# Performance work log

Measured on AMD Instinct MI355X. Metric: run time of the kernel, lower is better.

## Reference

```python
import jax, jax.numpy as jnp
import numpy as np

IN_F = 1024
OUT_F = 1024
GRID_SIZE = 8
GRID_LO, GRID_HI = -2.0, 2.0


def _grid_and_inv_denom():
    grid = jnp.linspace(GRID_LO, GRID_HI, GRID_SIZE)  # [G]
    inv_denom = 1.0 / (float((GRID_HI - GRID_LO) / (GRID_SIZE - 1)) + 1e-06)
    return grid, inv_denom


def setup_inputs() -> dict:
    key = jax.random.key(0)
    kx, kw, ks = jax.random.split(key, 3)
    x = jax.random.normal(kx, (4, 2048, IN_F), dtype=jnp.float32)
    # kaiming_uniform_(a=sqrt(5)) on [out,in]: bound = sqrt(6/((1+a^2)*fan_in)) = sqrt(1/fan_in)
    bound = float(np.sqrt(1.0 / IN_F))
    base_w = jax.random.uniform(kw, (OUT_F, IN_F), minval=-bound, maxval=bound, dtype=jnp.float32)
    base_b = jnp.zeros((OUT_F,), dtype=jnp.float32)
    spline_w = 0.02 * jax.random.normal(ks, (OUT_F, IN_F, GRID_SIZE), dtype=jnp.float32)
    return {"x": x, "base_w": base_w, "base_b": base_b, "spline_w": spline_w}


def reference(x, base_w, base_b, spline_w):
    grid, inv_denom = _grid_and_inv_denom()
    lead = x.shape[:-1]
    x_flat = x.reshape(-1, IN_F)  # [B, in]
    # base path: Linear(SiLU(x))
    base_out = jax.nn.silu(x_flat) @ base_w.T + base_b  # [B, out]
    # RBF basis expansion: [B, in, G]
    basis = jnp.exp(-(((x_flat[..., None] - grid) * inv_denom) ** 2))
    spline_out = jnp.einsum('big,oig->bo', basis, spline_w)  # [B, out]
    out = base_out + spline_out
    return out.reshape(*lead, OUT_F)
```

## Files before the change

kernel.cpp:

```cpp
#include <hip/hip_runtime.h>
#include <stdint.h>

namespace {

constexpr int IN_F = 1024;
constexpr int OUT_F = 1024;
constexpr int GSZ = 8;
constexpr int KTOT = IN_F + IN_F * GSZ;
constexpr int BK = 64;
constexpr int NT = KTOT / BK;
constexpr int NBASE = IN_F / BK;

constexpr int BM = 64, BN = 256;
constexpr int NBLK = OUT_F / BN;
constexpr size_t IMG_BYTES = (size_t)BN * BK * 2;
constexpr size_t WS_NEEDED = (size_t)NBLK * NT * IMG_BYTES;

constexpr double H_D     = 4.0 / 7.0;
constexpr double INVD_D  = 1.0 / (H_D + 1e-6);
constexpr double L2E_D   = 1.4426950408889634;
constexpr double SQL2E_D = 1.2011224087864498;
constexpr double CS_D    = INVD_D * SQL2E_D;
constexpr double DLT_D   = H_D * CS_D;

using short8 = __attribute__((ext_vector_type(8))) short;
using f32x4  = __attribute__((ext_vector_type(4))) float;

__device__ __forceinline__ unsigned cvt_pk(float lo, float hi) {
  unsigned r;
  asm("v_cvt_pk_bf16_f32 %0, %1, %2" : "=v"(r) : "v"(lo), "v"(hi));
  return r;
}
__device__ __forceinline__ float silu_f(float v) {
  float e = __builtin_amdgcn_exp2f(-v * (float)L2E_D);
  return v * __builtin_amdgcn_rcpf(1.0f + e);
}
__device__ __forceinline__ int swz(int row, int kk) {
  return (row * 128 + kk * 2) ^ ((row & 7) << 4);
}

__global__ void wprep(const float* __restrict__ bw, const float* __restrict__ sw,
                      char* __restrict__ wimg)
{
  const int total = NBLK * NT * BN * 8;
  for (int idx = blockIdx.x * blockDim.x + threadIdx.x; idx < total;
       idx += gridDim.x * blockDim.x) {
    const int kk8  = idx & 7;
    const int row  = (idx >> 3) & (BN - 1);
    const int rest = idx >> 11;
    const int step = rest % NT;
    const int nb   = rest / NT;
    const int o    = nb * BN + row;
    const int k    = step * BK + kk8 * 8;
    const float* src = (k < IN_F)
      ? (bw + (size_t)o * IN_F + k)
      : (sw + (size_t)o * (size_t)(IN_F * GSZ) + (k - IN_F));
    const float4 a = ((const float4*)src)[0];
    const float4 b = ((const float4*)src)[1];
    int4 v;
    v.x = (int)cvt_pk(a.x, a.y);
    v.y = (int)cvt_pk(a.z, a.w);
    v.z = (int)cvt_pk(b.x, b.y);
    v.w = (int)cvt_pk(b.z, b.w);
    *(int4*)(wimg + (size_t)rest * IMG_BYTES + swz(row, kk8 * 8)) = v;
  }
}

__global__ __launch_bounds__(256, 2)
void kan_fast(const float* __restrict__ x, const float* __restrict__ bb,
              const char* __restrict__ wimg, float* __restrict__ out)
{
  __shared__ char tA[2][BM * BK * 2];

  const int t    = threadIdx.x;
  const int lane = t & 63;
  const int wid  = t >> 6;
  const int wc   = wid * 64;

  const int d   = blockIdx.x;
  const int r8  = d & 7;
  const int nb  = r8 >> 1;
  const int my  = ((d >> 3) << 1) | (r8 & 1);
  const int bm0 = my * BM;
  const int bn0 = nb * BN;
  const char* img = wimg + (size_t)nb * NT * IMG_BYTES;

  const float CSf  = (float)CS_D;
  const float C0f  = (float)(-2.0 * CS_D);
  const float TDLT = (float)(2.0 * DLT_D);
  float Kc[7];
#pragma unroll
  for (int g = 0; g < 7; ++g) {
    const double cg  = (-2.0 + g * H_D) * CS_D;
    const double cg1 = (-2.0 + (g + 1) * H_D) * CS_D;
    Kc[g] = __builtin_amdgcn_exp2f((float)(-DLT_D * (cg + cg1)));
  }

  f32x4 acc[4][4];
#pragma unroll
  for (int m = 0; m < 4; ++m)
#pragma unroll
    for (int n = 0; n < 4; ++n) acc[m][n] = (f32x4)0.0f;

  const int fr = lane & 15;
  const int kq = (lane >> 4) * 8;

  int boff[8];
#pragma unroll
  for (int n = 0; n < 4; ++n)
#pragma unroll
    for (int kh = 0; kh < 2; ++kh)
      boff[n * 2 + kh] = swz(wc + n * 16 + fr, kh * 32 + kq);

  short8 bE[8], bO[8];
  float4 xE[4], xO[4];

  auto issue_B = [&](int step, short8 (&br)[8]) {
    const char* base = img + (size_t)step * IMG_BYTES;
#pragma unroll
    for (int j = 0; j < 8; ++j)
      br[j] = *(const short8*)(base + boff[j]);
  };

  const int prow = t >> 2;
  const int pcol = t & 3;

  auto load_x = [&](int step, float4 (&xr)[4]) {
    const int k0 = step * BK;
    if (k0 < IN_F) {
      const float* p = x + (size_t)(bm0 + prow) * IN_F + k0 + pcol * 16;
#pragma unroll
      for (int j = 0; j < 4; ++j) xr[j] = ((const float4*)p)[j];
    } else {
      const int i0 = (k0 - IN_F) >> 3;
      const float2 v = *(const float2*)(x + (size_t)(bm0 + prow) * IN_F + i0 + pcol * 2);
      xr[0].x = v.x; xr[0].y = v.y;
    }
  };

  auto conv_A = [&](int step, const float4 (&xr)[4], char* dstA) {
    if (step < NBASE) {
      unsigned q[8];
#pragma unroll
      for (int j = 0; j < 4; ++j) {
        q[2 * j]     = cvt_pk(silu_f(xr[j].x), silu_f(xr[j].y));
        q[2 * j + 1] = cvt_pk(silu_f(xr[j].z), silu_f(xr[j].w));
      }
      const int kc0 = pcol * 16;
      *(int4*)(dstA + swz(prow, kc0))     = make_int4(q[0], q[1], q[2], q[3]);
      *(int4*)(dstA + swz(prow, kc0 + 8)) = make_int4(q[4], q[5], q[6], q[7]);
    } else {
#pragma unroll
      for (int c = 0; c < 2; ++c) {
        const float xv = c ? xr[0].y : xr[0].x;
        const float tb = xv * CSf;
        const float d0 = tb - C0f;
        float e = __builtin_amdgcn_exp2f(-(d0 * d0));
        const float r = __builtin_amdgcn_exp2f(tb * TDLT);
        unsigned q[4];
#pragma unroll
        for (int g = 0; g < 4; ++g) {
          const float a = e;
          const float b = a * r * Kc[2 * g];
          q[g] = cvt_pk(a, b);
          if (g < 3) e = b * r * Kc[2 * g + 1];
        }
        *(int4*)(dstA + swz(prow, (pcol * 2 + c) * 8)) = make_int4(q[0], q[1], q[2], q[3]);
      }
    }
  };

  auto step_body = [&](int s, char* curA, char* nxtA,
                       short8 (&bCur)[8], short8 (&bNxt)[8],
                       const float4 (&xconv)[4], float4 (&xload)[4]) {
    if (s + 1 < NT) issue_B(s + 1, bNxt);
    if (s + 2 < NT) load_x(s + 2, xload);
    if (s + 1 < NT) conv_A(s + 1, xconv, nxtA);
    short8 af[4];
#pragma unroll
    for (int m = 0; m < 4; ++m)
      af[m] = *(const short8*)(curA + swz(m * 16 + fr, kq));
#pragma unroll
    for (int m = 0; m < 4; ++m)
#pragma unroll
      for (int n = 0; n < 4; ++n)
        acc[m][n] = __builtin_amdgcn_mfma_f32_16x16x32_bf16(af[m], bCur[n * 2], acc[m][n], 0, 0, 0);
#pragma unroll
    for (int m = 0; m < 4; ++m)
      af[m] = *(const short8*)(curA + swz(m * 16 + fr, 32 + kq));
#pragma unroll
    for (int m = 0; m < 4; ++m)
#pragma unroll
      for (int n = 0; n < 4; ++n)
        acc[m][n] = __builtin_amdgcn_mfma_f32_16x16x32_bf16(af[m], bCur[n * 2 + 1], acc[m][n], 0, 0, 0);
    __syncthreads();
  };

  load_x(0, xE);
  load_x(1, xO);
  issue_B(0, bE);
  conv_A(0, xE, tA[0]);
  __syncthreads();

  for (int s = 0; s < NT; s += 2) {
    step_body(s,     tA[0], tA[1], bE, bO, xO, xE);
    step_body(s + 1, tA[1], tA[0], bO, bE, xE, xO);
  }

  const int col = lane & 15;
  const int rr  = (lane >> 4) * 4;
#pragma unroll
  for (int m = 0; m < 4; ++m) {
    const int gr = bm0 + m * 16 + rr;
#pragma unroll
    for (int n = 0; n < 4; ++n) {
      const int gc = bn0 + wc + n * 16 + col;
      const float bias = bb[gc];
#pragma unroll
      for (int j = 0; j < 4; ++j)
        out[(size_t)(gr + j) * OUT_F + gc] = acc[m][n][j] + bias;
    }
  }
}

constexpr int SLDK = 64 + 8;

__device__ __forceinline__ unsigned f2bf(float f) {
  unsigned u = __float_as_uint(f);
  return (u + 0x7fffu + ((u >> 16) & 1u)) >> 16;
}
__device__ __forceinline__ unsigned pk2(float lo, float hi) {
  return f2bf(lo) | (f2bf(hi) << 16);
}

__global__ __launch_bounds__(256)
void kan_slow(const float* __restrict__ x, const float* __restrict__ bw,
              const float* __restrict__ bb, const float* __restrict__ sw,
              float* __restrict__ out)
{
  __shared__ unsigned short tA[128][SLDK];
  __shared__ unsigned short tB[128][SLDK];

  const int t    = threadIdx.x;
  const int lane = t & 63;
  const int wid  = t >> 6;
  const int wr   = (wid >> 1) * 64;
  const int wc   = (wid & 1) * 64;
  const int bm0  = blockIdx.x * 128;
  const int bn0  = blockIdx.y * 128;

  const float CS = (float)CS_D;
  float gsc[GSZ];
#pragma unroll
  for (int g = 0; g < GSZ; ++g)
    gsc[g] = (float)((-2.0 + g * H_D) * CS_D);

  f32x4 acc[4][4];
#pragma unroll
  for (int m = 0; m < 4; ++m)
#pragma unroll
    for (int n = 0; n < 4; ++n) acc[m][n] = (f32x4)0.0f;

  float4 rA[8], rB[8];
  const int rw = t >> 4;
  const int cw = (t & 15) * 4;

  auto load_tile = [&](int step) {
    const int k0 = step * BK;
    const bool base = (k0 < IN_F);
#pragma unroll
    for (int j = 0; j < 8; ++j) {
      const int row = j * 16 + rw;
      const float* p = base
        ? (bw + (size_t)(bn0 + row) * IN_F + k0 + cw)
        : (sw + (size_t)(bn0 + row) * (size_t)(IN_F * GSZ) + (k0 - IN_F) + cw);
      rB[j] = *(const float4*)p;
    }
    if (base) {
#pragma unroll
      for (int j = 0; j < 8; ++j) {
        const int row = j * 16 + rw;
        rA[j] = *(const float4*)(x + (size_t)(bm0 + row) * IN_F + k0 + cw);
      }
    } else {
      const int i0  = (k0 - IN_F) >> 3;
      const int row = t >> 1;
      rA[0] = *(const float4*)(x + (size_t)(bm0 + row) * IN_F + i0 + (t & 1) * 4);
    }
  };

  auto store_tile = [&](int step) {
    const int k0 = step * BK;
    const bool base = (k0 < IN_F);
#pragma unroll
    for (int j = 0; j < 8; ++j) {
      const int row = j * 16 + rw;
      uint2 v;
      v.x = pk2(rB[j].x, rB[j].y);
      v.y = pk2(rB[j].z, rB[j].w);
      *(uint2*)&tB[row][cw] = v;
    }
    if (base) {
#pragma unroll
      for (int j = 0; j < 8; ++j) {
        const int row = j * 16 + rw;
        uint2 v;
        v.x = pk2(silu_f(rA[j].x), silu_f(rA[j].y));
        v.y = pk2(silu_f(rA[j].z), silu_f(rA[j].w));
        *(uint2*)&tA[row][cw] = v;
      }
    } else {
      const int row  = t >> 1;
      const int half = t & 1;
      const float* xv = (const float*)&rA[0];
#pragma unroll
      for (int c = 0; c < 4; ++c) {
        const float tb = xv[c] * CS;
        union { unsigned u[4]; int4 v4; } pkv;
#pragma unroll
        for (int g = 0; g < 8; g += 2) {
          const float t0 = tb - gsc[g];
          const float t1 = tb - gsc[g + 1];
          const float e0 = __builtin_amdgcn_exp2f(-(t0 * t0));
          const float e1 = __builtin_amdgcn_exp2f(-(t1 * t1));
          pkv.u[g >> 1] = pk2(e0, e1);
        }
        const int kc = (half * 4 + c) * 8;
        *(int4*)&tA[row][kc] = pkv.v4;
      }
    }
  };

  auto compute_tile = [&]() {
    const int r  = lane & 15;
    const int kq = (lane >> 4) * 8;
#pragma unroll
    for (int kh = 0; kh < 2; ++kh) {
      short8 af[4], bf[4];
#pragma unroll
      for (int m = 0; m < 4; ++m)
        af[m] = *(const short8*)&tA[wr + m * 16 + r][kh * 32 + kq];
#pragma unroll
      for (int n = 0; n < 4; ++n)
        bf[n] = *(const short8*)&tB[wc + n * 16 + r][kh * 32 + kq];
#pragma unroll
      for (int m = 0; m < 4; ++m)
#pragma unroll
        for (int n = 0; n < 4; ++n)
          acc[m][n] = __builtin_amdgcn_mfma_f32_16x16x32_bf16(af[m], bf[n], acc[m][n], 0, 0, 0);
    }
  };

  load_tile(0);
  for (int step = 0; step < NT; ++step) {
    store_tile(step);
    __syncthreads();
    if (step + 1 < NT) load_tile(step + 1);
    compute_tile();
    __syncthreads();
  }

  const int col = lane & 15;
  const int rr  = (lane >> 4) * 4;
#pragma unroll
  for (int m = 0; m < 4; ++m) {
    const int gr = bm0 + wr + m * 16 + rr;
#pragma unroll
    for (int n = 0; n < 4; ++n) {
      const int gc = bn0 + wc + n * 16 + col;
      const float bias = bb[gc];
#pragma unroll
      for (int j = 0; j < 4; ++j)
        out[(size_t)(gr + j) * OUT_F + gc] = acc[m][n][j] + bias;
    }
  }
}

}

extern "C" void kernel_launch(void* const* d_in, const int* in_sizes, int n_in,
                              void* d_out, int out_size, void* d_ws, size_t ws_size,
                              hipStream_t stream) {
  const float *x, *bw, *bb, *sw;
  if (in_sizes[0] == OUT_F) {
    bb = (const float*)d_in[0];
    bw = (const float*)d_in[1];
    sw = (const float*)d_in[2];
    x  = (const float*)d_in[3];
  } else {
    x  = (const float*)d_in[0];
    bw = (const float*)d_in[1];
    bb = (const float*)d_in[2];
    sw = (const float*)d_in[3];
  }
  float* out = (float*)d_out;
  const int rows = (in_sizes[0] == OUT_F) ? in_sizes[3] / IN_F : in_sizes[0] / IN_F;

  if (ws_size >= WS_NEEDED && d_ws != nullptr && (rows % (2 * BM)) == 0) {
    hipLaunchKernelGGL(wprep, dim3(2048), dim3(256), 0, stream, bw, sw, (char*)d_ws);
    const int nblocks = NBLK * (rows / BM);
    hipLaunchKernelGGL(kan_fast, dim3(nblocks), dim3(256), 0, stream,
                       x, bb, (const char*)d_ws, out);
  } else {
    dim3 grid(rows / 128, OUT_F / 128);
    hipLaunchKernelGGL(kan_slow, grid, dim3(256), 0, stream, x, bw, bb, sw, out);
  }
}
```

Before: 191.2 us.

## Use 512-thread blocks with 8 waves each owning 32 output columns

Doubles threads per block to 512 and halves each wave's N tile from 64 to 32 columns. This cuts accumulator and B-register use so more waves can be resident per CU, with launch bounds of 4 blocks per CU. The A-tile conversion is split across twice as many threads, and the register double-buffering of B fragments is dropped in favor of loading B at the start of each step. It also raises wave priority with s_setprio around the MFMA section. In exchange, B-load latency is less hidden and each wave reuses its A fragments over fewer MFMAs, so LDS traffic per MFMA goes up.

```diff
diff --git a/kernel.cpp b/kernel.cpp
--- a/kernel.cpp
+++ b/kernel.cpp
@@ -66,7 +66,7 @@
   }
 }
 
-__global__ __launch_bounds__(256, 2)
+__global__ __launch_bounds__(512, 4)
 void kan_fast(const float* __restrict__ x, const float* __restrict__ bb,
               const char* __restrict__ wimg, float* __restrict__ out)
 {
@@ -75,7 +75,7 @@
   const int t    = threadIdx.x;
   const int lane = t & 63;
   const int wid  = t >> 6;
-  const int wc   = wid * 64;
+  const int wc   = wid * 32;
 
   const int d   = blockIdx.x;
   const int r8  = d & 7;
@@ -96,115 +96,109 @@
     Kc[g] = __builtin_amdgcn_exp2f((float)(-DLT_D * (cg + cg1)));
   }
 
-  f32x4 acc[4][4];
+  f32x4 acc[4][2];
 #pragma unroll
   for (int m = 0; m < 4; ++m)
 #pragma unroll
-    for (int n = 0; n < 4; ++n) acc[m][n] = (f32x4)0.0f;
+    for (int n = 0; n < 2; ++n) acc[m][n] = (f32x4)0.0f;
 
   const int fr = lane & 15;
   const int kq = (lane >> 4) * 8;
 
-  int boff[8];
-#pragma unroll
-  for (int n = 0; n < 4; ++n)
+  int boff[4];
+#pragma unroll
+  for (int n = 0; n < 2; ++n)
 #pragma unroll
     for (int kh = 0; kh < 2; ++kh)
       boff[n * 2 + kh] = swz(wc + n * 16 + fr, kh * 32 + kq);
-
-  short8 bE[8], bO[8];
-  float4 xE[4], xO[4];
-
-  auto issue_B = [&](int step, short8 (&br)[8]) {
-    const char* base = img + (size_t)step * IMG_BYTES;
-#pragma unroll
-    for (int j = 0; j < 8; ++j)
-      br[j] = *(const short8*)(base + boff[j]);
-  };
-
-  const int prow = t >> 2;
-  const int pcol = t & 3;
-
-  auto load_x = [&](int step, float4 (&xr)[4]) {
+  int aoff[8];
+#pragma unroll
+  for (int m = 0; m < 4; ++m)
+#pragma unroll
+    for (int kh = 0; kh < 2; ++kh)
+      aoff[m * 2 + kh] = swz(m * 16 + fr, kh * 32 + kq);
+
+  float4 xE[2], xO[2];
+
+  const int prow = t >> 3;
+  const int pcol = t & 7;
+
+  auto load_x = [&](int step, float4 (&xr)[2]) {
     const int k0 = step * BK;
     if (k0 < IN_F) {
-      const float* p = x + (size_t)(bm0 + prow) * IN_F + k0 + pcol * 16;
-#pragma unroll
-      for (int j = 0; j < 4; ++j) xr[j] = ((const float4*)p)[j];
+      const float* p = x + (size_t)(bm0 + prow) * IN_F + k0 + pcol * 8;
+      xr[0] = ((const float4*)p)[0];
+      xr[1] = ((const float4*)p)[1];
     } else {
       const int i0 = (k0 - IN_F) >> 3;
-      const float2 v = *(const float2*)(x + (size_t)(bm0 + prow) * IN_F + i0 + pcol * 2);
-      xr[0].x = v.x; xr[0].y = v.y;
-    }
-  };
-
-  auto conv_A = [&](int step, const float4 (&xr)[4], char* dstA) {
+      xr[0].x = x[(size_t)(bm0 + prow) * IN_F + i0 + pcol];
+    }
+  };
+
+  auto conv_A = [&](int step, const float4 (&xr)[2], char* dstA) {
+    char* dst = dstA + swz(prow, pcol * 8);
     if (step < NBASE) {
-      unsigned q[8];
-#pragma unroll
-      for (int j = 0; j < 4; ++j) {
-        q[2 * j]     = cvt_pk(silu_f(xr[j].x), silu_f(xr[j].y));
-        q[2 * j + 1] = cvt_pk(silu_f(xr[j].z), silu_f(xr[j].w));
+      unsigned q0 = cvt_pk(silu_f(xr[0].x), silu_f(xr[0].y));
+      unsigned q1 = cvt_pk(silu_f(xr[0].z), silu_f(xr[0].w));
+      unsigned q2 = cvt_pk(silu_f(xr[1].x), silu_f(xr[1].y));
+      unsigned q3 = cvt_pk(silu_f(xr[1].z), silu_f(xr[1].w));
+      *(int4*)dst = make_int4(q0, q1, q2, q3);
+    } else {
+      const float tb = xr[0].x * CSf;
+      const float d0 = tb - C0f;
+      float e = __builtin_amdgcn_exp2f(-(d0 * d0));
+      const float r = __builtin_amdgcn_exp2f(tb * TDLT);
+      unsigned q[4];
+#pragma unroll
+      for (int g = 0; g < 4; ++g) {
+        const float a = e;
+        const float b = a * r * Kc[2 * g];
+        q[g] = cvt_pk(a, b);
+        if (g < 3) e = b * r * Kc[2 * g + 1];
       }
-      const int kc0 = pcol * 16;
-      *(int4*)(dstA + swz(prow, kc0))     = make_int4(q[0], q[1], q[2], q[3]);
-      *(int4*)(dstA + swz(prow, kc0 + 8)) = make_int4(q[4], q[5], q[6], q[7]);
-    } else {
-#pragma unroll
-      for (int c = 0; c < 2; ++c) {
-        const float xv = c ? xr[0].y : xr[0].x;
-        const float tb = xv * CSf;
-        const float d0 = tb - C0f;
-        float e = __builtin_amdgcn_exp2f(-(d0 * d0));
-        const float r = __builtin_amdgcn_exp2f(tb * TDLT);
-        unsigned q[4];
-#pragma unroll
-        for (int g = 0; g < 4; ++g) {
-          const float a = e;
-          const float b = a * r * Kc[2 * g];
-          q[g] = cvt_pk(a, b);
-          if (g < 3) e = b * r * Kc[2 * g + 1];
-        }
-        *(int4*)(dstA + swz(prow, (pcol * 2 + c) * 8)) = make_int4(q[0], q[1], q[2], q[3]);
-      }
-    }
-  };
-
-  auto step_body = [&](int s, char* curA, char* nxtA,
-                       short8 (&bCur)[8], short8 (&bNxt)[8],
-                       const float4 (&xconv)[4], float4 (&xload)[4]) {
-    if (s + 1 < NT) issue_B(s + 1, bNxt);
+      *(int4*)dst = make_int4(q[0], q[1], q[2], q[3]);
+    }
+  };
+
+  auto step_body = [&](int s, const char* curA, char* nxtA,
+                       const float4 (&xconv)[2], float4 (&xload)[2]) {
+    short8 br[4];
+    const char* bbase = img + (size_t)s * IMG_BYTES;
+#pragma unroll
+    for (int j = 0; j < 4; ++j)
+      br[j] = *(const short8*)(bbase + boff[j]);
     if (s + 2 < NT) load_x(s + 2, xload);
     if (s + 1 < NT) conv_A(s + 1, xconv, nxtA);
     short8 af[4];
+    __builtin_amdgcn_s_setprio(1);
 #pragma unroll
     for (int m = 0; m < 4; ++m)
-      af[m] = *(const short8*)(curA + swz(m * 16 + fr, kq));
+      af[m] = *(const short8*)(curA + aoff[m * 2]);
 #pragma unroll
     for (int m = 0; m < 4; ++m)
 #pragma unroll
-      for (int n = 0; n < 4; ++n)
-        acc[m][n] = __builtin_amdgcn_mfma_f32_16x16x32_bf16(af[m], bCur[n * 2], acc[m][n], 0, 0, 0);
+      for (int n = 0; n < 2; ++n)
+        acc[m][n] = __builtin_amdgcn_mfma_f32_16x16x32_bf16(af[m], br[n * 2], acc[m][n], 0, 0, 0);
 #pragma unroll
     for (int m = 0; m < 4; ++m)
-      af[m] = *(const short8*)(curA + swz(m * 16 + fr, 32 + kq));
+      af[m] = *(const short8*)(curA + aoff[m * 2 + 1]);
 #pragma unroll
     for (int m = 0; m < 4; ++m)
 #pragma unroll
-      for (int n = 0; n < 4; ++n)
-        acc[m][n] = __builtin_amdgcn_mfma_f32_16x16x32_bf16(af[m], bCur[n * 2 + 1], acc[m][n], 0, 0, 0);
+      for (int n = 0; n < 2; ++n)
+        acc[m][n] = __builtin_amdgcn_mfma_f32_16x16x32_bf16(af[m], br[n * 2 + 1], acc[m][n], 0, 0, 0);
+    __builtin_amdgcn_s_setprio(0);
     __syncthreads();
   };
 
   load_x(0, xE);
   load_x(1, xO);
-  issue_B(0, bE);
   conv_A(0, xE, tA[0]);
   __syncthreads();
 
   for (int s = 0; s < NT; s += 2) {
-    step_body(s,     tA[0], tA[1], bE, bO, xO, xE);
-    step_body(s + 1, tA[1], tA[0], bO, bE, xE, xO);
+    step_body(s,     tA[0], tA[1], xO, xE);
+    step_body(s + 1, tA[1], tA[0], xE, xO);
   }
 
   const int col = lane & 15;
@@ -213,7 +207,7 @@
   for (int m = 0; m < 4; ++m) {
     const int gr = bm0 + m * 16 + rr;
 #pragma unroll
-    for (int n = 0; n < 4; ++n) {
+    for (int n = 0; n < 2; ++n) {
       const int gc = bn0 + wc + n * 16 + col;
       const float bias = bb[gc];
 #pragma unroll
@@ -399,7 +393,7 @@
   if (ws_size >= WS_NEEDED && d_ws != nullptr && (rows % (2 * BM)) == 0) {
     hipLaunchKernelGGL(wprep, dim3(2048), dim3(256), 0, stream, bw, sw, (char*)d_ws);
     const int nblocks = NBLK * (rows / BM);
-    hipLaunchKernelGGL(kan_fast, dim3(nblocks), dim3(256), 0, stream,
+    hipLaunchKernelGGL(kan_fast, dim3(nblocks), dim3(512), 0, stream,
                        x, bb, (const char*)d_ws, out);
   } else {
     dim3 grid(rows / 128, OUT_F / 128);
```

New measurement: 209.4 us. +9.5%, slower.

## Double block M tile to 128 with 8 waves and stage B in LDS via direct loads

Applied to the files above, without the earlier changes.

Raises the M tile to 128 rows and the block to 512 threads (2x4 waves), so each block reuses every weight tile for twice as many rows and total weight traffic is halved. B tiles now go straight into double-buffered LDS through global_load_lds instead of per-wave register loads. Hand-written waitcnt/barrier handling and setprio around the MFMA section replace __syncthreads to overlap loads with compute. In exchange LDS use grows, the grid holds half as many blocks, and correctness depends on the manual vmcnt counts matching the loads actually issued.

```diff
diff --git a/kernel.cpp b/kernel.cpp
--- a/kernel.cpp
+++ b/kernel.cpp
@@ -11,7 +11,7 @@
 constexpr int NT = KTOT / BK;
 constexpr int NBASE = IN_F / BK;
 
-constexpr int BM = 64, BN = 256;
+constexpr int BM = 128, BN = 256;
 constexpr int NBLK = OUT_F / BN;
 constexpr size_t IMG_BYTES = (size_t)BN * BK * 2;
 constexpr size_t WS_NEEDED = (size_t)NBLK * NT * IMG_BYTES;
@@ -66,21 +66,22 @@
   }
 }
 
-__global__ __launch_bounds__(256, 2)
+__global__ __launch_bounds__(512, 2)
 void kan_fast(const float* __restrict__ x, const float* __restrict__ bb,
               const char* __restrict__ wimg, float* __restrict__ out)
 {
   __shared__ char tA[2][BM * BK * 2];
+  __shared__ char tB[2][BN * BK * 2];
 
   const int t    = threadIdx.x;
   const int lane = t & 63;
   const int wid  = t >> 6;
-  const int wc   = wid * 64;
+  const int wr   = (wid >> 2) * 64;
+  const int wc   = (wid & 3) * 64;
 
   const int d   = blockIdx.x;
-  const int r8  = d & 7;
-  const int nb  = r8 >> 1;
-  const int my  = ((d >> 3) << 1) | (r8 & 1);
+  const int nb  = (d & 7) >> 1;
+  const int my  = ((d >> 3) << 1) | (d & 1);
   const int bm0 = my * BM;
   const int bn0 = nb * BN;
   const char* img = wimg + (size_t)nb * NT * IMG_BYTES;
@@ -104,26 +105,32 @@
 
   const int fr = lane & 15;
   const int kq = (lane >> 4) * 8;
-
-  int boff[8];
+  int aoff[8], boff[8];
+#pragma unroll
+  for (int m = 0; m < 4; ++m)
+#pragma unroll
+    for (int kh = 0; kh < 2; ++kh)
+      aoff[m * 2 + kh] = swz(wr + m * 16 + fr, kh * 32 + kq);
 #pragma unroll
   for (int n = 0; n < 4; ++n)
 #pragma unroll
     for (int kh = 0; kh < 2; ++kh)
       boff[n * 2 + kh] = swz(wc + n * 16 + fr, kh * 32 + kq);
 
-  short8 bE[8], bO[8];
   float4 xE[4], xO[4];
-
-  auto issue_B = [&](int step, short8 (&br)[8]) {
-    const char* base = img + (size_t)step * IMG_BYTES;
-#pragma unroll
-    for (int j = 0; j < 8; ++j)
-      br[j] = *(const short8*)(base + boff[j]);
-  };
 
   const int prow = t >> 2;
   const int pcol = t & 3;
+
+  auto issue_B = [&](int step, char* dstB) {
+    const char* g = img + (size_t)step * IMG_BYTES + t * 16;
+    char* l = dstB + t * 16;
+#pragma unroll
+    for (int j = 0; j < 4; ++j)
+      __builtin_amdgcn_global_load_lds(
+        (const __attribute__((address_space(1))) void*)(g + j * 8192),
+        (__attribute__((address_space(3))) void*)(l + j * 8192), 16, 0, 0);
+  };
 
   auto load_x = [&](int step, float4 (&xr)[4]) {
     const int k0 = step * BK;
@@ -170,48 +177,71 @@
     }
   };
 
-  auto step_body = [&](int s, char* curA, char* nxtA,
-                       short8 (&bCur)[8], short8 (&bNxt)[8],
+  auto step_body = [&](int s, const char* curA, const char* curB,
+                       char* nxtA, char* nxtB,
                        const float4 (&xconv)[4], float4 (&xload)[4]) {
-    if (s + 1 < NT) issue_B(s + 1, bNxt);
+    if (s + 1 < NT) issue_B(s + 1, nxtB);
+    __builtin_amdgcn_sched_barrier(0);
     if (s + 2 < NT) load_x(s + 2, xload);
+
+    short8 af0[4], af1[4], bf0[4], bf1[4];
+#pragma unroll
+    for (int m = 0; m < 4; ++m) {
+      af0[m] = *(const short8*)(curA + aoff[m * 2]);
+      af1[m] = *(const short8*)(curA + aoff[m * 2 + 1]);
+    }
+#pragma unroll
+    for (int n = 0; n < 4; ++n) {
+      bf0[n] = *(const short8*)(curB + boff[n * 2]);
+      bf1[n] = *(const short8*)(curB + boff[n * 2 + 1]);
+    }
+
     if (s + 1 < NT) conv_A(s + 1, xconv, nxtA);
-    short8 af[4];
+
+    __builtin_amdgcn_s_setprio(1);
 #pragma unroll
     for (int m = 0; m < 4; ++m)
-      af[m] = *(const short8*)(curA + swz(m * 16 + fr, kq));
+#pragma unroll
+      for (int n = 0; n < 4; ++n)
+        acc[m][n] = __builtin_amdgcn_mfma_f32_16x16x32_bf16(af0[m], bf0[n], acc[m][n], 0, 0, 0);
 #pragma unroll
     for (int m = 0; m < 4; ++m)
 #pragma unroll
       for (int n = 0; n < 4; ++n)
-        acc[m][n] = __builtin_amdgcn_mfma_f32_16x16x32_bf16(af[m], bCur[n * 2], acc[m][n], 0, 0, 0);
-#pragma unroll
-    for (int m = 0; m < 4; ++m)
-      af[m] = *(const short8*)(curA + swz(m * 16 + fr, 32 + kq));
-#pragma unroll
-    for (int m = 0; m < 4; ++m)
-#pragma unroll
-      for (int n = 0; n < 4; ++n)
-        acc[m][n] = __builtin_amdgcn_mfma_f32_16x16x32_bf16(af[m], bCur[n * 2 + 1], acc[m][n], 0, 0, 0);
-    __syncthreads();
+        acc[m][n] = __builtin_amdgcn_mfma_f32_16x16x32_bf16(af1[m], bf1[n], acc[m][n], 0, 0, 0);
+    __builtin_amdgcn_s_setprio(0);
+
+    if (s + 2 < NT) {
+      if (s + 2 < NBASE) {
+        asm volatile("s_waitcnt vmcnt(4) lgkmcnt(0)" ::: "memory");
+      } else {
+        asm volatile("s_waitcnt vmcnt(1) lgkmcnt(0)" ::: "memory");
+      }
+    } else {
+      asm volatile("s_waitcnt vmcnt(0) lgkmcnt(0)" ::: "memory");
+    }
+    __builtin_amdgcn_sched_barrier(0);
+    __builtin_amdgcn_s_barrier();
   };
 
   load_x(0, xE);
   load_x(1, xO);
-  issue_B(0, bE);
+  issue_B(0, tB[0]);
   conv_A(0, xE, tA[0]);
-  __syncthreads();
+  asm volatile("s_waitcnt vmcnt(0) lgkmcnt(0)" ::: "memory");
+  __builtin_amdgcn_sched_barrier(0);
+  __builtin_amdgcn_s_barrier();
 
   for (int s = 0; s < NT; s += 2) {
-    step_body(s,     tA[0], tA[1], bE, bO, xO, xE);
-    step_body(s + 1, tA[1], tA[0], bO, bE, xE, xO);
+    step_body(s,     tA[0], tB[0], tA[1], tB[1], xO, xE);
+    step_body(s + 1, tA[1], tB[1], tA[0], tB[0], xE, xO);
   }
 
   const int col = lane & 15;
   const int rr  = (lane >> 4) * 4;
 #pragma unroll
   for (int m = 0; m < 4; ++m) {
-    const int gr = bm0 + m * 16 + rr;
+    const int gr = bm0 + wr + m * 16 + rr;
 #pragma unroll
     for (int n = 0; n < 4; ++n) {
       const int gc = bn0 + wc + n * 16 + col;
@@ -399,7 +429,7 @@
   if (ws_size >= WS_NEEDED && d_ws != nullptr && (rows % (2 * BM)) == 0) {
     hipLaunchKernelGGL(wprep, dim3(2048), dim3(256), 0, stream, bw, sw, (char*)d_ws);
     const int nblocks = NBLK * (rows / BM);
-    hipLaunchKernelGGL(kan_fast, dim3(nblocks), dim3(256), 0, stream,
+    hipLaunchKernelGGL(kan_fast, dim3(nblocks), dim3(512), 0, stream,
                        x, bb, (const char*)d_ws, out);
   } else {
     dim3 grid(rows / 128, OUT_F / 128);
```

After: 203.4 us. 1.06x slower.
